# Kernel optimization log

Hardware: AMD Instinct MI355X
Metric: run time of the kernel (lower is better)

Reference implementation:

```python
import jax, jax.numpy as jnp
import numpy as np

R_MIN = 0.01
R_MAX = 0.6
H = 32            # polar radial bins (after pooling)
W = 64            # polar angular bins (after pooling)
UP_R = 10         # radial upsampling factor
UP_T = 10         # angular upsampling factor
ATT_ALPHA = 5.0
B, C, IMG = 64, 3, 224


def _conv(x, w, b):
    # NCHW valid conv, stride 1 (matches nn.Conv2d default padding=0)
    y = jax.lax.conv_general_dilated(x, w, (1, 1), 'VALID',
                                     dimension_numbers=('NCHW', 'OIHW', 'NCHW'))
    return y + b[None, :, None, None]


def _maxpool2(x):
    return jax.lax.reduce_window(x, -jnp.inf, jax.lax.max,
                                 (1, 1, 2, 2), (1, 1, 2, 2), 'VALID')


def _grid_sample_border(x, grid):
    # F.grid_sample, bilinear, padding_mode='border', align_corners=False
    Bn, Cn, Hi, Wi = x.shape
    ix = ((grid[..., 0] + 1.0) * Wi - 1.0) * 0.5   # x-coord -> width index
    iy = ((grid[..., 1] + 1.0) * Hi - 1.0) * 0.5   # y-coord -> height index
    x0f = jnp.floor(ix)
    y0f = jnp.floor(iy)
    wx = (ix - x0f)[..., None]
    wy = (iy - y0f)[..., None]
    x0 = jnp.clip(x0f.astype(jnp.int32), 0, Wi - 1)
    x1 = jnp.clip(x0f.astype(jnp.int32) + 1, 0, Wi - 1)
    y0 = jnp.clip(y0f.astype(jnp.int32), 0, Hi - 1)
    y1 = jnp.clip(y0f.astype(jnp.int32) + 1, 0, Hi - 1)
    bidx = jnp.arange(Bn)[:, None, None]
    v00 = x[bidx, :, y0, x0]   # [B,Hg,Wg,C]
    v01 = x[bidx, :, y0, x1]
    v10 = x[bidx, :, y1, x0]
    v11 = x[bidx, :, y1, x1]
    out = (v00 * (1 - wx) * (1 - wy) + v01 * wx * (1 - wy)
           + v10 * (1 - wx) * wy + v11 * wx * wy)
    return jnp.transpose(out, (0, 3, 1, 2))  # [B,C,Hg,Wg]


def setup_inputs() -> dict:
    key = jax.random.key(0)
    ks = jax.random.split(key, 10)
    x = jax.random.normal(ks[0], (B, C, IMG, IMG), dtype=jnp.float32)
    l_t_prev = jax.random.uniform(ks[1], (B, 2), dtype=jnp.float32)
    conv1_w = jax.random.normal(ks[2], (6, C, 5, 5), dtype=jnp.float32) * 0.1
    conv1_b = jnp.zeros((6,), jnp.float32)
    conv2_w = jax.random.normal(ks[3], (16, 6, 5, 5), dtype=jnp.float32) * 0.1
    conv2_b = jnp.zeros((16,), jnp.float32)
    fc1_w = jax.random.normal(ks[4], (8, 16), dtype=jnp.float32) * 0.1
    fc1_b = jnp.zeros((8,), jnp.float32)
    fc2_w = jax.random.normal(ks[5], (2, 8), dtype=jnp.float32) * 0.1
    fc2_b = jnp.zeros((2,), jnp.float32)
    return dict(x=x, l_t_prev=l_t_prev, conv1_w=conv1_w, conv1_b=conv1_b,
                conv2_w=conv2_w, conv2_b=conv2_b, fc1_w=fc1_w, fc1_b=fc1_b,
                fc2_w=fc2_w, fc2_b=fc2_b)


def reference(x, l_t_prev, conv1_w, conv1_b, conv2_w, conv2_b,
              fc1_w, fc1_b, fc2_w, fc2_b):
    # --- attention branch: conv -> maxpool -> conv -> GAP -> fc -> sigmoid ---
    h = _conv(x, conv1_w, conv1_b)
    h = _maxpool2(h)
    h = _conv(h, conv2_w, conv2_b)
    feat = h.mean(axis=(2, 3))                     # AdaptiveAvgPool2d(1), [B,16]
    h = jax.nn.relu(feat @ fc1_w.T + fc1_b)
    weight = jax.nn.sigmoid(h @ fc2_w.T + fc2_b) * ATT_ALPHA   # [B,2]
    # --- per-batch log-polar grid ---
    Hg, Wg = H * UP_R, W * UP_T
    angle = 2.0 * jnp.pi * jnp.arange(Wg, dtype=jnp.float32) / Wg
    unit = jnp.stack([jnp.sin(angle), jnp.cos(angle)], axis=-1)   # [Wg,2]
    start = jnp.log(R_MIN * weight[:, 0])
    stop = jnp.log(R_MAX * weight[:, 1])
    t = jnp.arange(Hg, dtype=jnp.float32) / (Hg - 1)
    radii = jnp.exp(start[:, None] + (stop - start)[:, None] * t[None])  # [B,Hg]
    grid = radii[:, :, None, None] * unit[None, None]     # [B,Hg,Wg,2]
    grid = grid + l_t_prev[:, None, None, :]
    # --- irregular bilinear sampling + box filter ---
    sampled = _grid_sample_border(x, grid)                 # [B,C,Hg,Wg]
    Bn, Cn = sampled.shape[:2]
    pooled = sampled.reshape(Bn, Cn, H, UP_R, W, UP_T).mean(axis=(3, 5))
    return pooled, weight
```

## Files before the change

### kernel.cpp

```cpp
#include <hip/hip_runtime.h>
#include <math.h>

#define Bn    64
#define Cn    3
#define IMG   224
#define PLANE (IMG*IMG)
#define C1    6
#define P1    110
#define P2    106
#define NVALID (P2*P2)
#define Hh    32
#define Ww    64
#define UPR   10
#define UPT   10
#define Hg    (Hh*UPR)
#define Wg    (Ww*UPT)
#define POOLED_SIZE (Bn*Cn*Hh*Ww)
#define NCHUNK 28
#define PSTRIDE 152
#define ROWB  (IMG*8)

typedef unsigned short u16;
typedef short s8v __attribute__((ext_vector_type(8)));
typedef float f4v __attribute__((ext_vector_type(4)));

#define PART_FLOATS ((size_t)Bn * NCHUNK * PSTRIDE)
#define X4B_U16     ((size_t)Bn * PLANE * 4)
#define WS_NEEDED   ((PART_FLOATS + Bn * 2) * 4 + X4B_U16 * 2)

__device__ __forceinline__ u16 f2bf(float f) {
    union { unsigned int u; float f; } c; c.f = f;
    unsigned int r = c.u + 0x7fffu + ((c.u >> 16) & 1u);
    return (u16)(r >> 16);
}
__device__ __forceinline__ float bf2f(u16 v) {
    union { unsigned int u; float f; } c; c.u = ((unsigned int)v) << 16;
    return c.f;
}

#define GSHFL(v, idx) __shfl((v), (lane & 48) + (idx), 64)

__global__ __launch_bounds__(256) void k1_fused(
    const float* __restrict__ x,
    const float* __restrict__ w1,
    const float* __restrict__ b1,
    float* __restrict__ partial,
    u16* __restrict__ x4b,
    int do_pack)
{
    __shared__ __attribute__((aligned(16))) unsigned char xs[12 * ROWB + 128];
    __shared__ float rowR[4][C1][4];
    __shared__ float edgeLo[4][C1][4];
    __shared__ float edgeHi[4][C1][4];

    const int b     = blockIdx.y;
    const int chunk = blockIdx.x;
    const int tid   = threadIdx.x;
    const int wid   = tid >> 6;
    const int lane  = tid & 63;
    const int n     = lane & 15;
    const int g     = lane >> 4;
    const int gy0   = chunk * 8;

    const float* xb = x + (size_t)b * (Cn * PLANE);

    s8v ahi[5], alo[5];
    #pragma unroll
    for (int ky = 0; ky < 5; ++ky) {
        #pragma unroll
        for (int j = 0; j < 8; ++j) {
            const int kmem = g * 8 + j;
            const int ic = kmem & 3, kx = kmem >> 2;
            float w = 0.0f;
            if (n < C1 && ic < 3 && kx < 5)
                w = w1[((n * 3 + ic) * 5 + ky) * 5 + kx];
            const u16 hb = f2bf(w);
            ahi[ky][j] = (short)hb;
            alo[ky][j] = (short)f2bf(w - bf2f(hb));
        }
    }
    f4v binit;
    #pragma unroll
    for (int e = 0; e < 4; ++e) {
        const int oc = g * 4 + e;
        binit[e] = (oc < C1) ? b1[oc] : 0.0f;
    }

    u16* ob = x4b + (size_t)b * PLANE * 4;
    for (int i = tid; i < 12 * 112; i += 256) {
        const int r = i / 112;
        const int p = i - r * 112;
        const int gy = gy0 + r;
        uint4 U; U.x = U.y = U.z = U.w = 0u;
        if (gy < IMG) {
            const float2 v0 = *(const float2*)(xb + 0 * PLANE + gy * IMG + 2 * p);
            const float2 v1 = *(const float2*)(xb + 1 * PLANE + gy * IMG + 2 * p);
            const float2 v2 = *(const float2*)(xb + 2 * PLANE + gy * IMG + 2 * p);
            U.x = (unsigned)f2bf(v0.x) | ((unsigned)f2bf(v1.x) << 16);
            U.y = (unsigned)f2bf(v2.x);
            U.z = (unsigned)f2bf(v0.y) | ((unsigned)f2bf(v1.y) << 16);
            U.w = (unsigned)f2bf(v2.y);
        }
        *(uint4*)(xs + r * ROWB + p * 16) = U;
        if (do_pack && r < 8)
            *(uint4*)(ob + ((size_t)gy * IMG + 2 * p) * 4) = U;
    }
    __syncthreads();

    float colsum[4][4];
    #pragma unroll
    for (int py = 0; py < 4; ++py)
        #pragma unroll
        for (int e = 0; e < 4; ++e) colsum[py][e] = 0.0f;

    for (int si = 0; si < 4; ++si) {
        const int s = wid + 4 * si;
        if (s >= 14) break;
        const unsigned sByte = (unsigned)(s * 128 + n * 8 + g * 16);

        f4v acc[8];
        #pragma unroll
        for (int q = 0; q < 8; ++q) acc[q] = binit;

        #pragma unroll
        for (int r = 0; r < 12; ++r) {
            s8v bf;
            const unsigned char* bp = xs + r * ROWB + sByte;
            ((unsigned long long*)&bf)[0] = *(const unsigned long long*)bp;
            ((unsigned long long*)&bf)[1] = *(const unsigned long long*)(bp + 8);
            #pragma unroll
            for (int ky = 0; ky < 5; ++ky) {
                const int q = r - ky;
                if (q >= 0 && q < 8)
                    acc[q] = __builtin_amdgcn_mfma_f32_16x16x32_bf16(
                        ahi[ky], bf, acc[q], 0, 0, 0);
            }
            #pragma unroll
            for (int ky = 0; ky < 5; ++ky) {
                const int q = r - ky;
                if (q >= 0 && q < 8)
                    acc[q] = __builtin_amdgcn_mfma_f32_16x16x32_bf16(
                        alo[ky], bf, acc[q], 0, 0, 0);
            }
        }

        #pragma unroll
        for (int py = 0; py < 4; ++py) {
            #pragma unroll
            for (int e = 0; e < 4; ++e) {
                float t = fmaxf(acc[2 * py][e], acc[2 * py + 1][e]);
                t = fmaxf(t, __shfl_xor(t, 1, 64));
                if (s == 13 && n >= 12) t = 0.0f;
                colsum[py][e] += t;
                const int oc = g * 4 + e;
                if (s == 0) {
                    const float c0 = GSHFL(t, 0), c1 = GSHFL(t, 2);
                    const float c2 = GSHFL(t, 4), c3 = GSHFL(t, 6);
                    const float S1 = c0, S2 = S1 + c1, S3 = S2 + c2, S4 = S3 + c3;
                    const float sv = (n == 0) ? S1 : (n == 1) ? S2 : (n == 2) ? S3 : S4;
                    if (n < 4 && oc < C1) edgeLo[py][oc][n] = sv;
                }
                if (s == 13) {
                    const float d109 = GSHFL(t, 10), d108 = GSHFL(t, 8);
                    const float d107 = GSHFL(t, 6),  d106 = GSHFL(t, 4);
                    const float U1 = d109, U2 = U1 + d108, U3 = U2 + d107, U4 = U3 + d106;
                    const float uv = (n == 0) ? U1 : (n == 1) ? U2 : (n == 2) ? U3 : U4;
                    if (n < 4 && oc < C1) edgeHi[py][oc][n] = uv;
                }
            }
        }
    }

    #pragma unroll
    for (int py = 0; py < 4; ++py) {
        #pragma unroll
        for (int e = 0; e < 4; ++e) {
            float v = colsum[py][e];
            v += __shfl_xor(v, 2, 64);
            v += __shfl_xor(v, 4, 64);
            v += __shfl_xor(v, 8, 64);
            const int oc = g * 4 + e;
            if (n == 0 && oc < C1) rowR[wid][oc][py] = v;
        }
    }
    __syncthreads();

    if (tid < 150) {
        const int oc = tid / 25;
        const int rem = tid - oc * 25;
        const int ky = rem / 5, kx = rem - ky * 5;
        float total = 0.0f;
        #pragma unroll
        for (int py = 0; py < 4; ++py) {
            const int y = chunk * 4 + py;
            const bool valid = (y < P1) && ((unsigned)(y - ky) <= 105u);
            float v = rowR[0][oc][py] + rowR[1][oc][py]
                    + rowR[2][oc][py] + rowR[3][oc][py];
            if (kx > 0) v -= edgeLo[py][oc][kx - 1];
            if (kx < 4) v -= edgeHi[py][oc][3 - kx];
            total += valid ? v : 0.0f;
        }
        partial[((size_t)b * NCHUNK + chunk) * PSTRIDE + tid] = total;
    }
}

__global__ __launch_bounds__(256) void k2_head(
    const float* __restrict__ partial, const float* __restrict__ w2,
    const float* __restrict__ b2, const float* __restrict__ fc1w,
    const float* __restrict__ fc1b, const float* __restrict__ fc2w,
    const float* __restrict__ fc2b, float* __restrict__ wt_ws,
    float* __restrict__ out)
{
    const int b = blockIdx.x;
    const int tid = threadIdx.x;
    __shared__ float wsb[150];
    __shared__ float sfeat[16];
    __shared__ float sh[8];

    if (tid < 150) {
        const float* p = partial + (size_t)b * NCHUNK * PSTRIDE + tid;
        float s = 0.0f;
        #pragma unroll
        for (int c = 0; c < NCHUNK; ++c) s += p[c * PSTRIDE];
        wsb[tid] = s;
    }
    __syncthreads();
    if (tid < 16) {
        float s = 0.0f;
        for (int j = 0; j < 150; ++j) s += w2[tid * 150 + j] * wsb[j];
        sfeat[tid] = b2[tid] + s * (1.0f / (float)NVALID);
    }
    __syncthreads();
    if (tid < 8) {
        float s = fc1b[tid];
        #pragma unroll
        for (int j = 0; j < 16; ++j) s += fc1w[tid * 16 + j] * sfeat[j];
        sh[tid] = fmaxf(s, 0.0f);
    }
    __syncthreads();
    if (tid < 2) {
        float s = fc2b[tid];
        #pragma unroll
        for (int j = 0; j < 8; ++j) s += fc2w[tid * 8 + j] * sh[j];
        float sig = (s >= 0.0f) ? (1.0f / (1.0f + expf(-s)))
                                : (expf(s) / (1.0f + expf(s)));
        const float wgt = 5.0f * sig;
        wt_ws[b * 2 + tid] = wgt;
        out[POOLED_SIZE + b * 2 + tid] = wgt;
    }
}

__device__ __forceinline__ void sample_coords(
    float gxn, float gyn, int& x0, int& y0, float& wx, float& wy)
{
    float ix = ((gxn + 1.0f) * (float)IMG - 1.0f) * 0.5f;
    float iy = ((gyn + 1.0f) * (float)IMG - 1.0f) * 0.5f;
    ix = fminf(fmaxf(ix, 0.0f), (float)(IMG - 1));
    iy = fminf(fmaxf(iy, 0.0f), (float)(IMG - 1));
    x0 = (int)ix; if (x0 > IMG - 2) x0 = IMG - 2;
    y0 = (int)iy; if (y0 > IMG - 2) y0 = IMG - 2;
    wx = ix - (float)x0;
    wy = iy - (float)y0;
}

__global__ __launch_bounds__(640) void k3_sample_pool_bf16(
    const u16* __restrict__ x4b,
    const float* __restrict__ ltp,
    const float* __restrict__ wt,
    float* __restrict__ out)
{
    __shared__ float part[3 * Wg];

    const int L = blockIdx.x;
    const int q = L >> 3;
    const int h = q & 31;
    const int b = (L & 7) + 8 * (q >> 5);
    const int tid = threadIdx.x;

    const float w0 = wt[b * 2 + 0];
    const float w1 = wt[b * 2 + 1];
    const float l0 = ltp[b * 2 + 0];
    const float l1 = ltp[b * 2 + 1];
    const float start = logf(0.01f * w0);
    const float stop  = logf(0.6f  * w1);
    const float dr = stop - start;

    const float angle = 6.283185307179586f * (float)tid / (float)Wg;
    const float sn = sinf(angle);
    const float cs = cosf(angle);

    const u16* xb4 = x4b + (size_t)b * PLANE * 4;

    const float ratio = expf(dr * (1.0f / (float)(Hg - 1)));
    float r = expf(start + dr * ((float)(h * UPR) / (float)(Hg - 1)));

    float acc0 = 0.0f, acc1 = 0.0f, acc2 = 0.0f;
    #pragma unroll
    for (int i = 0; i < UPR; ++i) {
        int x0, y0; float wx, wy;
        sample_coords(r * sn + l0, r * cs + l1, x0, y0, wx, wy);
        r *= ratio;

        const u16* base = xb4 + ((size_t)(y0 * IMG + x0)) * 4;
        const ushort4 a00 = *(const ushort4*)(base);
        const ushort4 a01 = *(const ushort4*)(base + 4);
        const ushort4 a10 = *(const ushort4*)(base + IMG * 4);
        const ushort4 a11 = *(const ushort4*)(base + IMG * 4 + 4);

        const float wx0 = 1.0f - wx, wy0 = 1.0f - wy;
        const float w00 = wx0 * wy0, w01 = wx * wy0;
        const float w10 = wx0 * wy,  w11 = wx * wy;

        acc0 += w00*bf2f(a00.x) + w01*bf2f(a01.x) + w10*bf2f(a10.x) + w11*bf2f(a11.x);
        acc1 += w00*bf2f(a00.y) + w01*bf2f(a01.y) + w10*bf2f(a10.y) + w11*bf2f(a11.y);
        acc2 += w00*bf2f(a00.z) + w01*bf2f(a01.z) + w10*bf2f(a10.z) + w11*bf2f(a11.z);
    }
    part[0 * Wg + tid] = acc0;
    part[1 * Wg + tid] = acc1;
    part[2 * Wg + tid] = acc2;
    __syncthreads();

    if (tid < Cn * Ww) {
        const int c = tid / Ww;
        const int w = tid % Ww;
        const float* p = part + c * Wg + w * UPT;
        float s = 0.0f;
        #pragma unroll
        for (int j = 0; j < UPT; ++j) s += p[j];
        out[(((size_t)b * Cn + c) * Hh + h) * Ww + w] = s * (1.0f / (UPR * UPT));
    }
}

__global__ __launch_bounds__(640) void k3_sample_pool_nchw(
    const float* __restrict__ x, const float* __restrict__ ltp,
    const float* __restrict__ wt, float* __restrict__ out)
{
    __shared__ float part[3 * Wg];
    const int L = blockIdx.x;
    const int q = L >> 3;
    const int h = q & 31;
    const int b = (L & 7) + 8 * (q >> 5);
    const int tid = threadIdx.x;

    const float w0 = wt[b * 2 + 0];
    const float w1 = wt[b * 2 + 1];
    const float l0 = ltp[b * 2 + 0];
    const float l1 = ltp[b * 2 + 1];
    const float start = logf(0.01f * w0);
    const float stop  = logf(0.6f  * w1);
    const float dr = stop - start;
    const float angle = 6.283185307179586f * (float)tid / (float)Wg;
    const float sn = sinf(angle);
    const float cs = cosf(angle);
    const float* xb = x + (size_t)b * Cn * PLANE;

    const float ratio = expf(dr * (1.0f / (float)(Hg - 1)));
    float r = expf(start + dr * ((float)(h * UPR) / (float)(Hg - 1)));

    float acc0 = 0.0f, acc1 = 0.0f, acc2 = 0.0f;
    #pragma unroll
    for (int i = 0; i < UPR; ++i) {
        int x0, y0; float wx, wy;
        sample_coords(r * sn + l0, r * cs + l1, x0, y0, wx, wy);
        r *= ratio;
        const float wx0 = 1.0f - wx, wy0 = 1.0f - wy;
        const float w00 = wx0 * wy0, w01 = wx * wy0;
        const float w10 = wx0 * wy,  w11 = wx * wy;
        const int o00 = y0 * IMG + x0;
        acc0 += w00*xb[o00] + w01*xb[o00+1] + w10*xb[o00+IMG] + w11*xb[o00+IMG+1];
        const float* x1p = xb + PLANE;
        acc1 += w00*x1p[o00] + w01*x1p[o00+1] + w10*x1p[o00+IMG] + w11*x1p[o00+IMG+1];
        const float* x2p = xb + 2 * PLANE;
        acc2 += w00*x2p[o00] + w01*x2p[o00+1] + w10*x2p[o00+IMG] + w11*x2p[o00+IMG+1];
    }
    part[0 * Wg + tid] = acc0;
    part[1 * Wg + tid] = acc1;
    part[2 * Wg + tid] = acc2;
    __syncthreads();

    if (tid < Cn * Ww) {
        const int c = tid / Ww;
        const int w = tid % Ww;
        const float* p = part + c * Wg + w * UPT;
        float s = 0.0f;
        #pragma unroll
        for (int j = 0; j < UPT; ++j) s += p[j];
        out[(((size_t)b * Cn + c) * Hh + h) * Ww + w] = s * (1.0f / (UPR * UPT));
    }
}

extern "C" void kernel_launch(void* const* d_in, const int* in_sizes, int n_in,
                              void* d_out, int out_size, void* d_ws, size_t ws_size,
                              hipStream_t stream) {
    const float* x       = (const float*)d_in[0];
    const float* ltp     = (const float*)d_in[1];
    const float* conv1_w = (const float*)d_in[2];
    const float* conv1_b = (const float*)d_in[3];
    const float* conv2_w = (const float*)d_in[4];
    const float* conv2_b = (const float*)d_in[5];
    const float* fc1_w   = (const float*)d_in[6];
    const float* fc1_b   = (const float*)d_in[7];
    const float* fc2_w   = (const float*)d_in[8];
    const float* fc2_b   = (const float*)d_in[9];
    float* out = (float*)d_out;

    const int do_pack = (ws_size >= WS_NEEDED) ? 1 : 0;

    float* part_ws = (float*)d_ws;
    float* wt_ws   = part_ws + PART_FLOATS;
    u16*   x4b     = (u16*)(wt_ws + Bn * 2);

    k1_fused<<<dim3(NCHUNK, Bn), dim3(256), 0, stream>>>(
        x, conv1_w, conv1_b, part_ws, x4b, do_pack);
    k2_head<<<dim3(Bn), dim3(256), 0, stream>>>(part_ws, conv2_w, conv2_b,
                                                fc1_w, fc1_b, fc2_w, fc2_b,
                                                wt_ws, out);
    if (do_pack)
        k3_sample_pool_bf16<<<dim3(Hh * Bn), dim3(Wg), 0, stream>>>(x4b, ltp, wt_ws, out);
    else
        k3_sample_pool_nchw<<<dim3(Hh * Bn), dim3(Wg), 0, stream>>>(x, ltp, wt_ws, out);
}
```

Baseline: 175.7 us.

## Switch conv1 to single-pass fp16 MFMA, widen blocks, fuse head into sampler

Conv1 now uses single fp16 MFMAs instead of a bf16 hi/lo split, which halves the MFMA count, and the packed image cache moves from bf16 to fp16. k1 grows to 448 threads (7 waves, 2 strips each), with wave 0 staging weights in LDS while the other waves load the tile. The k2 head kernel is removed and its reduction plus FC layers are recomputed redundantly in every k3 block, which saves a launch but repeats the head work per block. Fast __sinf/__cosf and a single 16-byte load per row pair replace the previous calls and loads. fp16 narrows the input range relative to bf16/fp32 and may change accuracy.

```diff
diff --git a/kernel.cpp b/kernel.cpp
--- a/kernel.cpp
+++ b/kernel.cpp
@@ -19,37 +19,42 @@
 #define NCHUNK 28
 #define PSTRIDE 152
 #define ROWB  (IMG*8)
+#define TPB1  448
 
 typedef unsigned short u16;
-typedef short s8v __attribute__((ext_vector_type(8)));
+typedef unsigned long long ull;
+typedef _Float16 h8v __attribute__((ext_vector_type(8)));
 typedef float f4v __attribute__((ext_vector_type(4)));
 
 #define PART_FLOATS ((size_t)Bn * NCHUNK * PSTRIDE)
 #define X4B_U16     ((size_t)Bn * PLANE * 4)
 #define WS_NEEDED   ((PART_FLOATS + Bn * 2) * 4 + X4B_U16 * 2)
 
-__device__ __forceinline__ u16 f2bf(float f) {
-    union { unsigned int u; float f; } c; c.f = f;
-    unsigned int r = c.u + 0x7fffu + ((c.u >> 16) & 1u);
-    return (u16)(r >> 16);
-}
-__device__ __forceinline__ float bf2f(u16 v) {
-    union { unsigned int u; float f; } c; c.u = ((unsigned int)v) << 16;
-    return c.f;
+__device__ __forceinline__ unsigned hpack(float a, float b) {
+    union { _Float16 h; u16 u; } x, y;
+    x.h = (_Float16)a; y.h = (_Float16)b;
+    return (unsigned)x.u | ((unsigned)y.u << 16);
+}
+__device__ __forceinline__ float h2lo(unsigned v) {
+    union { _Float16 h; u16 u; } c; c.u = (u16)(v & 0xffffu); return (float)c.h;
+}
+__device__ __forceinline__ float h2hi(unsigned v) {
+    union { _Float16 h; u16 u; } c; c.u = (u16)(v >> 16); return (float)c.h;
 }
 
 #define GSHFL(v, idx) __shfl((v), (lane & 48) + (idx), 64)
 
-__global__ __launch_bounds__(256) void k1_fused(
+__global__ __launch_bounds__(TPB1) void k1_fused(
     const float* __restrict__ x,
     const float* __restrict__ w1,
     const float* __restrict__ b1,
     float* __restrict__ partial,
-    u16* __restrict__ x4b,
+    u16* __restrict__ x4h,
     int do_pack)
 {
     __shared__ __attribute__((aligned(16))) unsigned char xs[12 * ROWB + 128];
-    __shared__ float rowR[4][C1][4];
+    __shared__ __attribute__((aligned(16))) _Float16 sa[5][64][8];
+    __shared__ float rowR[7][C1][4];
     __shared__ float edgeLo[4][C1][4];
     __shared__ float edgeHi[4][C1][4];
 
@@ -63,22 +68,46 @@
     const int gy0   = chunk * 8;
 
     const float* xb = x + (size_t)b * (Cn * PLANE);
-
-    s8v ahi[5], alo[5];
-    #pragma unroll
-    for (int ky = 0; ky < 5; ++ky) {
-        #pragma unroll
-        for (int j = 0; j < 8; ++j) {
-            const int kmem = g * 8 + j;
-            const int ic = kmem & 3, kx = kmem >> 2;
-            float w = 0.0f;
-            if (n < C1 && ic < 3 && kx < 5)
-                w = w1[((n * 3 + ic) * 5 + ky) * 5 + kx];
-            const u16 hb = f2bf(w);
-            ahi[ky][j] = (short)hb;
-            alo[ky][j] = (short)f2bf(w - bf2f(hb));
-        }
-    }
+    u16* ob = x4h + (size_t)b * PLANE * 4;
+
+    if (wid == 0) {
+        #pragma unroll
+        for (int ky = 0; ky < 5; ++ky) {
+            #pragma unroll
+            for (int j = 0; j < 8; ++j) {
+                const int kmem = g * 8 + j;
+                const int ic = kmem & 3, kx = kmem >> 2;
+                float w = 0.0f;
+                if (n < C1 && ic < 3 && kx < 5)
+                    w = w1[((n * 3 + ic) * 5 + ky) * 5 + kx];
+                sa[ky][lane][j] = (_Float16)w;
+            }
+        }
+    } else {
+        for (int i = tid - 64; i < 12 * 112; i += TPB1 - 64) {
+            const int r = i / 112;
+            const int p = i - r * 112;
+            const int gy = gy0 + r;
+            uint4 U; U.x = U.y = U.z = U.w = 0u;
+            if (gy < IMG) {
+                const float2 v0 = *(const float2*)(xb + 0 * PLANE + gy * IMG + 2 * p);
+                const float2 v1 = *(const float2*)(xb + 1 * PLANE + gy * IMG + 2 * p);
+                const float2 v2 = *(const float2*)(xb + 2 * PLANE + gy * IMG + 2 * p);
+                U.x = hpack(v0.x, v1.x);
+                U.y = hpack(v2.x, 0.0f);
+                U.z = hpack(v0.y, v1.y);
+                U.w = hpack(v2.y, 0.0f);
+            }
+            *(uint4*)(xs + r * ROWB + p * 16) = U;
+            if (do_pack && r < 8)
+                *(uint4*)(ob + ((size_t)gy * IMG + 2 * p) * 4) = U;
+        }
+    }
+    __syncthreads();
+
+    h8v a[5];
+    #pragma unroll
+    for (int ky = 0; ky < 5; ++ky) a[ky] = *(const h8v*)&sa[ky][lane][0];
     f4v binit;
     #pragma unroll
     for (int e = 0; e < 4; ++e) {
@@ -86,36 +115,15 @@
         binit[e] = (oc < C1) ? b1[oc] : 0.0f;
     }
 
-    u16* ob = x4b + (size_t)b * PLANE * 4;
-    for (int i = tid; i < 12 * 112; i += 256) {
-        const int r = i / 112;
-        const int p = i - r * 112;
-        const int gy = gy0 + r;
-        uint4 U; U.x = U.y = U.z = U.w = 0u;
-        if (gy < IMG) {
-            const float2 v0 = *(const float2*)(xb + 0 * PLANE + gy * IMG + 2 * p);
-            const float2 v1 = *(const float2*)(xb + 1 * PLANE + gy * IMG + 2 * p);
-            const float2 v2 = *(const float2*)(xb + 2 * PLANE + gy * IMG + 2 * p);
-            U.x = (unsigned)f2bf(v0.x) | ((unsigned)f2bf(v1.x) << 16);
-            U.y = (unsigned)f2bf(v2.x);
-            U.z = (unsigned)f2bf(v0.y) | ((unsigned)f2bf(v1.y) << 16);
-            U.w = (unsigned)f2bf(v2.y);
-        }
-        *(uint4*)(xs + r * ROWB + p * 16) = U;
-        if (do_pack && r < 8)
-            *(uint4*)(ob + ((size_t)gy * IMG + 2 * p) * 4) = U;
-    }
-    __syncthreads();
-
     float colsum[4][4];
     #pragma unroll
     for (int py = 0; py < 4; ++py)
         #pragma unroll
         for (int e = 0; e < 4; ++e) colsum[py][e] = 0.0f;
 
-    for (int si = 0; si < 4; ++si) {
-        const int s = wid + 4 * si;
-        if (s >= 14) break;
+    #pragma unroll
+    for (int si = 0; si < 2; ++si) {
+        const int s = wid * 2 + si;
         const unsigned sByte = (unsigned)(s * 128 + n * 8 + g * 16);
 
         f4v acc[8];
@@ -124,23 +132,16 @@
 
         #pragma unroll
         for (int r = 0; r < 12; ++r) {
-            s8v bf;
+            h8v bf;
             const unsigned char* bp = xs + r * ROWB + sByte;
-            ((unsigned long long*)&bf)[0] = *(const unsigned long long*)bp;
-            ((unsigned long long*)&bf)[1] = *(const unsigned long long*)(bp + 8);
+            ((ull*)&bf)[0] = *(const ull*)bp;
+            ((ull*)&bf)[1] = *(const ull*)(bp + 8);
             #pragma unroll
             for (int ky = 0; ky < 5; ++ky) {
                 const int q = r - ky;
                 if (q >= 0 && q < 8)
-                    acc[q] = __builtin_amdgcn_mfma_f32_16x16x32_bf16(
-                        ahi[ky], bf, acc[q], 0, 0, 0);
-            }
-            #pragma unroll
-            for (int ky = 0; ky < 5; ++ky) {
-                const int q = r - ky;
-                if (q >= 0 && q < 8)
-                    acc[q] = __builtin_amdgcn_mfma_f32_16x16x32_bf16(
-                        alo[ky], bf, acc[q], 0, 0, 0);
+                    acc[q] = __builtin_amdgcn_mfma_f32_16x16x32_f16(
+                        a[ky], bf, acc[q], 0, 0, 0);
             }
         }
 
@@ -194,8 +195,9 @@
         for (int py = 0; py < 4; ++py) {
             const int y = chunk * 4 + py;
             const bool valid = (y < P1) && ((unsigned)(y - ky) <= 105u);
-            float v = rowR[0][oc][py] + rowR[1][oc][py]
-                    + rowR[2][oc][py] + rowR[3][oc][py];
+            float v = rowR[0][oc][py] + rowR[1][oc][py] + rowR[2][oc][py]
+                    + rowR[3][oc][py] + rowR[4][oc][py] + rowR[5][oc][py]
+                    + rowR[6][oc][py];
             if (kx > 0) v -= edgeLo[py][oc][kx - 1];
             if (kx < 4) v -= edgeHi[py][oc][3 - kx];
             total += valid ? v : 0.0f;
@@ -204,51 +206,39 @@
     }
 }
 
-__global__ __launch_bounds__(256) void k2_head(
-    const float* __restrict__ partial, const float* __restrict__ w2,
-    const float* __restrict__ b2, const float* __restrict__ fc1w,
-    const float* __restrict__ fc1b, const float* __restrict__ fc2w,
-    const float* __restrict__ fc2b, float* __restrict__ wt_ws,
-    float* __restrict__ out)
-{
-    const int b = blockIdx.x;
-    const int tid = threadIdx.x;
-    __shared__ float wsb[150];
-    __shared__ float sfeat[16];
-    __shared__ float sh[8];
-
-    if (tid < 150) {
-        const float* p = partial + (size_t)b * NCHUNK * PSTRIDE + tid;
-        float s = 0.0f;
-        #pragma unroll
-        for (int c = 0; c < NCHUNK; ++c) s += p[c * PSTRIDE];
-        wsb[tid] = s;
-    }
+#define K3_HEAD_BODY                                                          \
+    if (tid < 150) {                                                          \
+        const float* p = partial + (size_t)b * NCHUNK * PSTRIDE + tid;        \
+        float s = 0.0f;                                                       \
+        _Pragma("unroll")                                                     \
+        for (int c = 0; c < NCHUNK; ++c) s += p[c * PSTRIDE];                 \
+        wsb[tid] = s;                                                         \
+    }                                                                         \
+    __syncthreads();                                                          \
+    if (tid < 16) {                                                           \
+        float s = 0.0f;                                                       \
+        for (int j = 0; j < 150; ++j) s += w2[tid * 150 + j] * wsb[j];        \
+        sfeat[tid] = b2[tid] + s * (1.0f / (float)NVALID);                    \
+    }                                                                         \
+    __syncthreads();                                                          \
+    if (tid < 8) {                                                            \
+        float s = fc1b[tid];                                                  \
+        _Pragma("unroll")                                                     \
+        for (int j = 0; j < 16; ++j) s += fc1w[tid * 16 + j] * sfeat[j];      \
+        sh[tid] = fmaxf(s, 0.0f);                                             \
+    }                                                                         \
+    __syncthreads();                                                          \
+    if (tid < 2) {                                                            \
+        float s = fc2b[tid];                                                  \
+        _Pragma("unroll")                                                     \
+        for (int j = 0; j < 8; ++j) s += fc2w[tid * 8 + j] * sh[j];           \
+        float sig = (s >= 0.0f) ? (1.0f / (1.0f + expf(-s)))                  \
+                                : (expf(s) / (1.0f + expf(s)));               \
+        const float wgt = 5.0f * sig;                                         \
+        sWt[tid] = wgt;                                                       \
+        out[POOLED_SIZE + b * 2 + tid] = wgt;                                 \
+    }                                                                         \
     __syncthreads();
-    if (tid < 16) {
-        float s = 0.0f;
-        for (int j = 0; j < 150; ++j) s += w2[tid * 150 + j] * wsb[j];
-        sfeat[tid] = b2[tid] + s * (1.0f / (float)NVALID);
-    }
-    __syncthreads();
-    if (tid < 8) {
-        float s = fc1b[tid];
-        #pragma unroll
-        for (int j = 0; j < 16; ++j) s += fc1w[tid * 16 + j] * sfeat[j];
-        sh[tid] = fmaxf(s, 0.0f);
-    }
-    __syncthreads();
-    if (tid < 2) {
-        float s = fc2b[tid];
-        #pragma unroll
-        for (int j = 0; j < 8; ++j) s += fc2w[tid * 8 + j] * sh[j];
-        float sig = (s >= 0.0f) ? (1.0f / (1.0f + expf(-s)))
-                                : (expf(s) / (1.0f + expf(s)));
-        const float wgt = 5.0f * sig;
-        wt_ws[b * 2 + tid] = wgt;
-        out[POOLED_SIZE + b * 2 + tid] = wgt;
-    }
-}
 
 __device__ __forceinline__ void sample_coords(
     float gxn, float gyn, int& x0, int& y0, float& wx, float& wy)
@@ -263,13 +253,20 @@
     wy = iy - (float)y0;
 }
 
-__global__ __launch_bounds__(640) void k3_sample_pool_bf16(
-    const u16* __restrict__ x4b,
+__global__ __launch_bounds__(640) void k3_sample_pool_f16(
+    const u16* __restrict__ x4h,
     const float* __restrict__ ltp,
-    const float* __restrict__ wt,
+    const float* __restrict__ partial,
+    const float* __restrict__ w2,  const float* __restrict__ b2,
+    const float* __restrict__ fc1w, const float* __restrict__ fc1b,
+    const float* __restrict__ fc2w, const float* __restrict__ fc2b,
     float* __restrict__ out)
 {
     __shared__ float part[3 * Wg];
+    __shared__ float wsb[150];
+    __shared__ float sfeat[16];
+    __shared__ float sh[8];
+    __shared__ float sWt[2];
 
     const int L = blockIdx.x;
     const int q = L >> 3;
@@ -277,8 +274,10 @@
     const int b = (L & 7) + 8 * (q >> 5);
     const int tid = threadIdx.x;
 
-    const float w0 = wt[b * 2 + 0];
-    const float w1 = wt[b * 2 + 1];
+    K3_HEAD_BODY
+
+    const float w0 = sWt[0];
+    const float w1 = sWt[1];
     const float l0 = ltp[b * 2 + 0];
     const float l1 = ltp[b * 2 + 1];
     const float start = logf(0.01f * w0);
@@ -286,10 +285,10 @@
     const float dr = stop - start;
 
     const float angle = 6.283185307179586f * (float)tid / (float)Wg;
-    const float sn = sinf(angle);
-    const float cs = cosf(angle);
-
-    const u16* xb4 = x4b + (size_t)b * PLANE * 4;
+    const float sn = __sinf(angle);
+    const float cs = __cosf(angle);
+
+    const u16* xb4 = x4h + (size_t)b * PLANE * 4;
 
     const float ratio = expf(dr * (1.0f / (float)(Hg - 1)));
     float r = expf(start + dr * ((float)(h * UPR) / (float)(Hg - 1)));
@@ -302,18 +301,16 @@
         r *= ratio;
 
         const u16* base = xb4 + ((size_t)(y0 * IMG + x0)) * 4;
-        const ushort4 a00 = *(const ushort4*)(base);
-        const ushort4 a01 = *(const ushort4*)(base + 4);
-        const ushort4 a10 = *(const ushort4*)(base + IMG * 4);
-        const ushort4 a11 = *(const ushort4*)(base + IMG * 4 + 4);
+        const uint4 R0 = *(const uint4*)(base);
+        const uint4 R1 = *(const uint4*)(base + IMG * 4);
 
         const float wx0 = 1.0f - wx, wy0 = 1.0f - wy;
         const float w00 = wx0 * wy0, w01 = wx * wy0;
         const float w10 = wx0 * wy,  w11 = wx * wy;
 
-        acc0 += w00*bf2f(a00.x) + w01*bf2f(a01.x) + w10*bf2f(a10.x) + w11*bf2f(a11.x);
-        acc1 += w00*bf2f(a00.y) + w01*bf2f(a01.y) + w10*bf2f(a10.y) + w11*bf2f(a11.y);
-        acc2 += w00*bf2f(a00.z) + w01*bf2f(a01.z) + w10*bf2f(a10.z) + w11*bf2f(a11.z);
+        acc0 += w00*h2lo(R0.x) + w01*h2lo(R0.z) + w10*h2lo(R1.x) + w11*h2lo(R1.z);
+        acc1 += w00*h2hi(R0.x) + w01*h2hi(R0.z) + w10*h2hi(R1.x) + w11*h2hi(R1.z);
+        acc2 += w00*h2lo(R0.y) + w01*h2lo(R0.w) + w10*h2lo(R1.y) + w11*h2lo(R1.w);
     }
     part[0 * Wg + tid] = acc0;
     part[1 * Wg + tid] = acc1;
@@ -333,25 +330,36 @@
 
 __global__ __launch_bounds__(640) void k3_sample_pool_nchw(
     const float* __restrict__ x, const float* __restrict__ ltp,
-    const float* __restrict__ wt, float* __restrict__ out)
+    const float* __restrict__ partial,
+    const float* __restrict__ w2,  const float* __restrict__ b2,
+    const float* __restrict__ fc1w, const float* __restrict__ fc1b,
+    const float* __restrict__ fc2w, const float* __restrict__ fc2b,
+    float* __restrict__ out)
 {
     __shared__ float part[3 * Wg];
+    __shared__ float wsb[150];
+    __shared__ float sfeat[16];
+    __shared__ float sh[8];
+    __shared__ float sWt[2];
+
     const int L = blockIdx.x;
     const int q = L >> 3;
     const int h = q & 31;
     const int b = (L & 7) + 8 * (q >> 5);
     const int tid = threadIdx.x;
 
-    const float w0 = wt[b * 2 + 0];
-    const float w1 = wt[b * 2 + 1];
+    K3_HEAD_BODY
+
+    const float w0 = sWt[0];
+    const float w1 = sWt[1];
     const float l0 = ltp[b * 2 + 0];
     const float l1 = ltp[b * 2 + 1];
     const float start = logf(0.01f * w0);
     const float stop  = logf(0.6f  * w1);
     const float dr = stop - start;
     const float angle = 6.283185307179586f * (float)tid / (float)Wg;
-    const float sn = sinf(angle);
-    const float cs = cosf(angle);
+    const float sn = __sinf(angle);
+    const float cs = __cosf(angle);
     const float* xb = x + (size_t)b * Cn * PLANE;
 
     const float ratio = expf(dr * (1.0f / (float)(Hg - 1)));
@@ -407,16 +415,16 @@
     const int do_pack = (ws_size >= WS_NEEDED) ? 1 : 0;
 
     float* part_ws = (float*)d_ws;
-    float* wt_ws   = part_ws + PART_FLOATS;
-    u16*   x4b     = (u16*)(wt_ws + Bn * 2);
-
-    k1_fused<<<dim3(NCHUNK, Bn), dim3(256), 0, stream>>>(
-        x, conv1_w, conv1_b, part_ws, x4b, do_pack);
-    k2_head<<<dim3(Bn), dim3(256), 0, stream>>>(part_ws, conv2_w, conv2_b,
-                                                fc1_w, fc1_b, fc2_w, fc2_b,
-                                                wt_ws, out);
+    u16*   x4h     = (u16*)(part_ws + PART_FLOATS + Bn * 2);
+
+    k1_fused<<<dim3(NCHUNK, Bn), dim3(TPB1), 0, stream>>>(
+        x, conv1_w, conv1_b, part_ws, x4h, do_pack);
     if (do_pack)
-        k3_sample_pool_bf16<<<dim3(Hh * Bn), dim3(Wg), 0, stream>>>(x4b, ltp, wt_ws, out);
+        k3_sample_pool_f16<<<dim3(Hh * Bn), dim3(Wg), 0, stream>>>(
+            x4h, ltp, part_ws, conv2_w, conv2_b,
+            fc1_w, fc1_b, fc2_w, fc2_b, out);
     else
-        k3_sample_pool_nchw<<<dim3(Hh * Bn), dim3(Wg), 0, stream>>>(x, ltp, wt_ws, out);
-}
+        k3_sample_pool_nchw<<<dim3(Hh * Bn), dim3(Wg), 0, stream>>>(
+            x, ltp, part_ws, conv2_w, conv2_b,
+            fc1_w, fc1_b, fc2_w, fc2_b, out);
+}
```

Result: slower. 184.9 us (+5.3%).

## Switch conv1 to single-pass fp16 MFMA and process two chunks per block

Applied to the files above, without the earlier changes.

Conv1 now runs a single fp16 MFMA pass instead of split bf16 hi/lo passes, which halves the matrix work. The packed image copy used for sampling is stored as fp16. Each block of 448 threads handles two row chunks with 7 waves, and it prefetches the second chunk's global loads into registers while the first chunk is computing. The conv weights are staged through shared memory, the sampler fetches each row pair with one 16-byte load, and sin/cos use the fast intrinsics. The risks are lower precision from the single fp16 pass, fp16 range issues, and reduced occupancy from the larger register and shared-memory footprint.

```diff
diff --git a/kernel.cpp b/kernel.cpp
--- a/kernel.cpp
+++ b/kernel.cpp
@@ -19,103 +19,46 @@
 #define NCHUNK 28
 #define PSTRIDE 152
 #define ROWB  (IMG*8)
+#define TPB1  448
 
 typedef unsigned short u16;
-typedef short s8v __attribute__((ext_vector_type(8)));
+typedef unsigned long long ull;
+typedef _Float16 h8v __attribute__((ext_vector_type(8)));
 typedef float f4v __attribute__((ext_vector_type(4)));
 
 #define PART_FLOATS ((size_t)Bn * NCHUNK * PSTRIDE)
 #define X4B_U16     ((size_t)Bn * PLANE * 4)
 #define WS_NEEDED   ((PART_FLOATS + Bn * 2) * 4 + X4B_U16 * 2)
 
-__device__ __forceinline__ u16 f2bf(float f) {
-    union { unsigned int u; float f; } c; c.f = f;
-    unsigned int r = c.u + 0x7fffu + ((c.u >> 16) & 1u);
-    return (u16)(r >> 16);
-}
-__device__ __forceinline__ float bf2f(u16 v) {
-    union { unsigned int u; float f; } c; c.u = ((unsigned int)v) << 16;
-    return c.f;
+__device__ __forceinline__ unsigned hpack(float a, float b) {
+    union { _Float16 h; u16 u; } x, y;
+    x.h = (_Float16)a; y.h = (_Float16)b;
+    return (unsigned)x.u | ((unsigned)y.u << 16);
+}
+__device__ __forceinline__ float h2lo(unsigned v) {
+    union { _Float16 h; u16 u; } c; c.u = (u16)(v & 0xffffu); return (float)c.h;
+}
+__device__ __forceinline__ float h2hi(unsigned v) {
+    union { _Float16 h; u16 u; } c; c.u = (u16)(v >> 16); return (float)c.h;
 }
 
 #define GSHFL(v, idx) __shfl((v), (lane & 48) + (idx), 64)
 
-__global__ __launch_bounds__(256) void k1_fused(
-    const float* __restrict__ x,
-    const float* __restrict__ w1,
-    const float* __restrict__ b1,
-    float* __restrict__ partial,
-    u16* __restrict__ x4b,
-    int do_pack)
-{
-    __shared__ __attribute__((aligned(16))) unsigned char xs[12 * ROWB + 128];
-    __shared__ float rowR[4][C1][4];
-    __shared__ float edgeLo[4][C1][4];
-    __shared__ float edgeHi[4][C1][4];
-
-    const int b     = blockIdx.y;
-    const int chunk = blockIdx.x;
-    const int tid   = threadIdx.x;
-    const int wid   = tid >> 6;
-    const int lane  = tid & 63;
-    const int n     = lane & 15;
-    const int g     = lane >> 4;
-    const int gy0   = chunk * 8;
-
-    const float* xb = x + (size_t)b * (Cn * PLANE);
-
-    s8v ahi[5], alo[5];
-    #pragma unroll
-    for (int ky = 0; ky < 5; ++ky) {
-        #pragma unroll
-        for (int j = 0; j < 8; ++j) {
-            const int kmem = g * 8 + j;
-            const int ic = kmem & 3, kx = kmem >> 2;
-            float w = 0.0f;
-            if (n < C1 && ic < 3 && kx < 5)
-                w = w1[((n * 3 + ic) * 5 + ky) * 5 + kx];
-            const u16 hb = f2bf(w);
-            ahi[ky][j] = (short)hb;
-            alo[ky][j] = (short)f2bf(w - bf2f(hb));
-        }
-    }
-    f4v binit;
-    #pragma unroll
-    for (int e = 0; e < 4; ++e) {
-        const int oc = g * 4 + e;
-        binit[e] = (oc < C1) ? b1[oc] : 0.0f;
-    }
-
-    u16* ob = x4b + (size_t)b * PLANE * 4;
-    for (int i = tid; i < 12 * 112; i += 256) {
-        const int r = i / 112;
-        const int p = i - r * 112;
-        const int gy = gy0 + r;
-        uint4 U; U.x = U.y = U.z = U.w = 0u;
-        if (gy < IMG) {
-            const float2 v0 = *(const float2*)(xb + 0 * PLANE + gy * IMG + 2 * p);
-            const float2 v1 = *(const float2*)(xb + 1 * PLANE + gy * IMG + 2 * p);
-            const float2 v2 = *(const float2*)(xb + 2 * PLANE + gy * IMG + 2 * p);
-            U.x = (unsigned)f2bf(v0.x) | ((unsigned)f2bf(v1.x) << 16);
-            U.y = (unsigned)f2bf(v2.x);
-            U.z = (unsigned)f2bf(v0.y) | ((unsigned)f2bf(v1.y) << 16);
-            U.w = (unsigned)f2bf(v2.y);
-        }
-        *(uint4*)(xs + r * ROWB + p * 16) = U;
-        if (do_pack && r < 8)
-            *(uint4*)(ob + ((size_t)gy * IMG + 2 * p) * 4) = U;
-    }
-    __syncthreads();
-
+__device__ __forceinline__ void conv_chunk(
+    const unsigned char* xs, const h8v* a, f4v binit,
+    int wid, int lane, int n, int g, int tid, int chunk,
+    float (*rowR)[C1][4], float (*edgeLo)[C1][4], float (*edgeHi)[C1][4],
+    float* __restrict__ partial_slot)
+{
     float colsum[4][4];
     #pragma unroll
     for (int py = 0; py < 4; ++py)
         #pragma unroll
         for (int e = 0; e < 4; ++e) colsum[py][e] = 0.0f;
 
-    for (int si = 0; si < 4; ++si) {
-        const int s = wid + 4 * si;
-        if (s >= 14) break;
+    #pragma unroll
+    for (int si = 0; si < 2; ++si) {
+        const int s = wid * 2 + si;
         const unsigned sByte = (unsigned)(s * 128 + n * 8 + g * 16);
 
         f4v acc[8];
@@ -124,23 +67,16 @@
 
         #pragma unroll
         for (int r = 0; r < 12; ++r) {
-            s8v bf;
+            h8v bf;
             const unsigned char* bp = xs + r * ROWB + sByte;
-            ((unsigned long long*)&bf)[0] = *(const unsigned long long*)bp;
-            ((unsigned long long*)&bf)[1] = *(const unsigned long long*)(bp + 8);
+            ((ull*)&bf)[0] = *(const ull*)bp;
+            ((ull*)&bf)[1] = *(const ull*)(bp + 8);
             #pragma unroll
             for (int ky = 0; ky < 5; ++ky) {
                 const int q = r - ky;
                 if (q >= 0 && q < 8)
-                    acc[q] = __builtin_amdgcn_mfma_f32_16x16x32_bf16(
-                        ahi[ky], bf, acc[q], 0, 0, 0);
-            }
-            #pragma unroll
-            for (int ky = 0; ky < 5; ++ky) {
-                const int q = r - ky;
-                if (q >= 0 && q < 8)
-                    acc[q] = __builtin_amdgcn_mfma_f32_16x16x32_bf16(
-                        alo[ky], bf, acc[q], 0, 0, 0);
+                    acc[q] = __builtin_amdgcn_mfma_f32_16x16x32_f16(
+                        a[ky], bf, acc[q], 0, 0, 0);
             }
         }
 
@@ -194,14 +130,129 @@
         for (int py = 0; py < 4; ++py) {
             const int y = chunk * 4 + py;
             const bool valid = (y < P1) && ((unsigned)(y - ky) <= 105u);
-            float v = rowR[0][oc][py] + rowR[1][oc][py]
-                    + rowR[2][oc][py] + rowR[3][oc][py];
+            float v = rowR[0][oc][py] + rowR[1][oc][py] + rowR[2][oc][py]
+                    + rowR[3][oc][py] + rowR[4][oc][py] + rowR[5][oc][py]
+                    + rowR[6][oc][py];
             if (kx > 0) v -= edgeLo[py][oc][kx - 1];
             if (kx < 4) v -= edgeHi[py][oc][3 - kx];
             total += valid ? v : 0.0f;
         }
-        partial[((size_t)b * NCHUNK + chunk) * PSTRIDE + tid] = total;
-    }
+        partial_slot[tid] = total;
+    }
+}
+
+__global__ __launch_bounds__(TPB1) void k1_fused(
+    const float* __restrict__ x,
+    const float* __restrict__ w1,
+    const float* __restrict__ b1,
+    float* __restrict__ partial,
+    u16* __restrict__ x4h,
+    int do_pack)
+{
+    __shared__ __attribute__((aligned(16))) unsigned char xs[12 * ROWB + 128];
+    __shared__ __attribute__((aligned(16))) _Float16 sa[5][64][8];
+    __shared__ float rowR[7][C1][4];
+    __shared__ float edgeLo[4][C1][4];
+    __shared__ float edgeHi[4][C1][4];
+
+    const int l    = blockIdx.x;
+    const int b    = (l & 7) + 8 * ((l >> 3) & 7);
+    const int cp   = l >> 6;
+    const int chunk0 = 2 * cp, chunk1 = 2 * cp + 1;
+    const int gy00 = chunk0 * 8, gy01 = chunk1 * 8;
+    const int tid  = threadIdx.x;
+    const int wid  = tid >> 6;
+    const int lane = tid & 63;
+    const int n    = lane & 15;
+    const int g    = lane >> 4;
+
+    const float* xb = x + (size_t)b * (Cn * PLANE);
+    u16* ob = x4h + (size_t)b * PLANE * 4;
+
+    if (wid == 0) {
+        #pragma unroll
+        for (int ky = 0; ky < 5; ++ky) {
+            #pragma unroll
+            for (int j = 0; j < 8; ++j) {
+                const int kmem = g * 8 + j;
+                const int ic = kmem & 3, kx = kmem >> 2;
+                float w = 0.0f;
+                if (n < C1 && ic < 3 && kx < 5)
+                    w = w1[((n * 3 + ic) * 5 + ky) * 5 + kx];
+                sa[ky][lane][j] = (_Float16)w;
+            }
+        }
+    } else {
+        for (int i = tid - 64; i < 12 * 112; i += TPB1 - 64) {
+            const int r = i / 112;
+            const int p = i - r * 112;
+            const int gy = gy00 + r;
+            uint4 U; U.x = U.y = U.z = U.w = 0u;
+            if (gy < IMG) {
+                const float2 v0 = *(const float2*)(xb + 0 * PLANE + gy * IMG + 2 * p);
+                const float2 v1 = *(const float2*)(xb + 1 * PLANE + gy * IMG + 2 * p);
+                const float2 v2 = *(const float2*)(xb + 2 * PLANE + gy * IMG + 2 * p);
+                U.x = hpack(v0.x, v1.x);
+                U.y = hpack(v2.x, 0.0f);
+                U.z = hpack(v0.y, v1.y);
+                U.w = hpack(v2.y, 0.0f);
+            }
+            *(uint4*)(xs + r * ROWB + p * 16) = U;
+            if (do_pack && r < 8)
+                *(uint4*)(ob + ((size_t)gy * IMG + 2 * p) * 4) = U;
+        }
+    }
+    __syncthreads();
+
+    h8v a[5];
+    #pragma unroll
+    for (int ky = 0; ky < 5; ++ky) a[ky] = *(const h8v*)&sa[ky][lane][0];
+    f4v binit;
+    #pragma unroll
+    for (int e = 0; e < 4; ++e) {
+        const int oc = g * 4 + e;
+        binit[e] = (oc < C1) ? b1[oc] : 0.0f;
+    }
+
+    float2 rv0[3], rv1[3], rv2[3];
+    #pragma unroll
+    for (int k = 0; k < 3; ++k) {
+        const int i = tid + k * TPB1;
+        const int r = i / 112, p = i - r * 112;
+        const int gy = gy01 + r;
+        float2 z; z.x = 0.0f; z.y = 0.0f;
+        rv0[k] = z; rv1[k] = z; rv2[k] = z;
+        if (gy < IMG) {
+            rv0[k] = *(const float2*)(xb + 0 * PLANE + gy * IMG + 2 * p);
+            rv1[k] = *(const float2*)(xb + 1 * PLANE + gy * IMG + 2 * p);
+            rv2[k] = *(const float2*)(xb + 2 * PLANE + gy * IMG + 2 * p);
+        }
+    }
+
+    conv_chunk(xs, a, binit, wid, lane, n, g, tid, chunk0,
+               rowR, edgeLo, edgeHi,
+               partial + ((size_t)b * NCHUNK + chunk0) * PSTRIDE);
+    __syncthreads();
+
+    #pragma unroll
+    for (int k = 0; k < 3; ++k) {
+        const int i = tid + k * TPB1;
+        const int r = i / 112, p = i - r * 112;
+        uint4 U;
+        U.x = hpack(rv0[k].x, rv1[k].x);
+        U.y = hpack(rv2[k].x, 0.0f);
+        U.z = hpack(rv0[k].y, rv1[k].y);
+        U.w = hpack(rv2[k].y, 0.0f);
+        *(uint4*)(xs + r * ROWB + p * 16) = U;
+        const int gy = gy01 + r;
+        if (do_pack && r < 8 && gy < IMG)
+            *(uint4*)(ob + ((size_t)gy * IMG + 2 * p) * 4) = U;
+    }
+    __syncthreads();
+
+    conv_chunk(xs, a, binit, wid, lane, n, g, tid, chunk1,
+               rowR, edgeLo, edgeHi,
+               partial + ((size_t)b * NCHUNK + chunk1) * PSTRIDE);
 }
 
 __global__ __launch_bounds__(256) void k2_head(
@@ -263,8 +314,8 @@
     wy = iy - (float)y0;
 }
 
-__global__ __launch_bounds__(640) void k3_sample_pool_bf16(
-    const u16* __restrict__ x4b,
+__global__ __launch_bounds__(640) void k3_sample_pool_f16(
+    const u16* __restrict__ x4h,
     const float* __restrict__ ltp,
     const float* __restrict__ wt,
     float* __restrict__ out)
@@ -286,10 +337,10 @@
     const float dr = stop - start;
 
     const float angle = 6.283185307179586f * (float)tid / (float)Wg;
-    const float sn = sinf(angle);
-    const float cs = cosf(angle);
-
-    const u16* xb4 = x4b + (size_t)b * PLANE * 4;
+    const float sn = __sinf(angle);
+    const float cs = __cosf(angle);
+
+    const u16* xb4 = x4h + (size_t)b * PLANE * 4;
 
     const float ratio = expf(dr * (1.0f / (float)(Hg - 1)));
     float r = expf(start + dr * ((float)(h * UPR) / (float)(Hg - 1)));
@@ -302,18 +353,16 @@
         r *= ratio;
 
         const u16* base = xb4 + ((size_t)(y0 * IMG + x0)) * 4;
-        const ushort4 a00 = *(const ushort4*)(base);
-        const ushort4 a01 = *(const ushort4*)(base + 4);
-        const ushort4 a10 = *(const ushort4*)(base + IMG * 4);
-        const ushort4 a11 = *(const ushort4*)(base + IMG * 4 + 4);
+        const uint4 R0 = *(const uint4*)(base);
+        const uint4 R1 = *(const uint4*)(base + IMG * 4);
 
         const float wx0 = 1.0f - wx, wy0 = 1.0f - wy;
         const float w00 = wx0 * wy0, w01 = wx * wy0;
         const float w10 = wx0 * wy,  w11 = wx * wy;
 
-        acc0 += w00*bf2f(a00.x) + w01*bf2f(a01.x) + w10*bf2f(a10.x) + w11*bf2f(a11.x);
-        acc1 += w00*bf2f(a00.y) + w01*bf2f(a01.y) + w10*bf2f(a10.y) + w11*bf2f(a11.y);
-        acc2 += w00*bf2f(a00.z) + w01*bf2f(a01.z) + w10*bf2f(a10.z) + w11*bf2f(a11.z);
+        acc0 += w00*h2lo(R0.x) + w01*h2lo(R0.z) + w10*h2lo(R1.x) + w11*h2lo(R1.z);
+        acc1 += w00*h2hi(R0.x) + w01*h2hi(R0.z) + w10*h2hi(R1.x) + w11*h2hi(R1.z);
+        acc2 += w00*h2lo(R0.y) + w01*h2lo(R0.w) + w10*h2lo(R1.y) + w11*h2lo(R1.w);
     }
     part[0 * Wg + tid] = acc0;
     part[1 * Wg + tid] = acc1;
@@ -350,8 +399,8 @@
     const float stop  = logf(0.6f  * w1);
     const float dr = stop - start;
     const float angle = 6.283185307179586f * (float)tid / (float)Wg;
-    const float sn = sinf(angle);
-    const float cs = cosf(angle);
+    const float sn = __sinf(angle);
+    const float cs = __cosf(angle);
     const float* xb = x + (size_t)b * Cn * PLANE;
 
     const float ratio = expf(dr * (1.0f / (float)(Hg - 1)));
@@ -408,15 +457,15 @@
 
     float* part_ws = (float*)d_ws;
     float* wt_ws   = part_ws + PART_FLOATS;
-    u16*   x4b     = (u16*)(wt_ws + Bn * 2);
-
-    k1_fused<<<dim3(NCHUNK, Bn), dim3(256), 0, stream>>>(
-        x, conv1_w, conv1_b, part_ws, x4b, do_pack);
+    u16*   x4h     = (u16*)(wt_ws + Bn * 2);
+
+    k1_fused<<<dim3(Bn * NCHUNK / 2), dim3(TPB1), 0, stream>>>(
+        x, conv1_w, conv1_b, part_ws, x4h, do_pack);
     k2_head<<<dim3(Bn), dim3(256), 0, stream>>>(part_ws, conv2_w, conv2_b,
                                                 fc1_w, fc1_b, fc2_w, fc2_b,
                                                 wt_ws, out);
     if (do_pack)
-        k3_sample_pool_bf16<<<dim3(Hh * Bn), dim3(Wg), 0, stream>>>(x4b, ltp, wt_ws, out);
+        k3_sample_pool_f16<<<dim3(Hh * Bn), dim3(Wg), 0, stream>>>(x4h, ltp, wt_ws, out);
     else
         k3_sample_pool_nchw<<<dim3(Hh * Bn), dim3(Wg), 0, stream>>>(x, ltp, wt_ws, out);
 }
```

New measurement: 179.0 us. No clear change (+1.9%).
